# Performance work log

Measured on AMD Instinct MI355X. Metric: run time of the kernel, lower is better.

## Reference

```python
import jax, jax.numpy as jnp
import numpy as np

B, L, D, H = 2, 1000, 288, 8
DIM = D // H          # 36 per-head dim
DFF = 2 * D           # 576 conv-FFN hidden
KS = L // 4           # 250 sampled keys per query
NQ = L // 4           # 250 selected (active) queries
EPS = 1e-5


def _layernorm(x, g, b):
    mu = x.mean(-1, keepdims=True)
    var = ((x - mu) ** 2).mean(-1, keepdims=True)
    return (x - mu) * jax.lax.rsqrt(var + EPS) * g + b


def _prob_attention(q, k, v, index_key):
    # q,k,v: [b,h,L,dim]; index_key: [L, KS]
    b, h, l, dim = q.shape
    # sample KS keys per query row (gather): [b,h,L,KS,dim]
    k_samp = jnp.take(k, index_key, axis=2)
    # sampled scores: [b,h,L,KS]
    scores_samp = jnp.einsum('bhld,bhlkd->bhlk', q, k_samp)
    # sparsity measure M(q) = max - mean(over full l_key, as in source)
    measure = scores_samp.max(-1) - scores_samp.sum(-1) / l
    # top-NQ active queries per (b,h): [b,h,NQ]
    idx_q = jax.lax.top_k(measure, NQ)[1]
    q_sel = jnp.take_along_axis(q, idx_q[..., None], axis=2)  # [b,h,NQ,dim]
    sim = jnp.einsum('bhqd,bhkd->bhqk', q_sel, k) * (1.0 / np.sqrt(dim))
    attn = jax.nn.softmax(sim, axis=-1)
    out_sel = jnp.einsum('bhqk,bhkd->bhqd', attn, v)          # [b,h,NQ,dim]
    # lazy queries get mean(V); scatter active outputs in
    out = jnp.broadcast_to(v.mean(axis=2, keepdims=True), v.shape)
    bi = jnp.arange(b)[:, None, None]
    hi = jnp.arange(h)[None, :, None]
    out = out.at[bi, hi, idx_q].set(out_sel)
    return out  # [b,h,L,dim]


def reference(x, index_key, Wq, bq, Wk, bk, Wv, bv, W1, b1, W2, b2,
              ln1_g, ln1_b, ln2_g, ln2_b):
    b, l, d = x.shape
    # QKV projections -> [b,h,L,dim]
    q = (x @ Wq.T + bq).reshape(b, l, H, DIM).transpose(0, 2, 1, 3)
    k = (x @ Wk.T + bk).reshape(b, l, H, DIM).transpose(0, 2, 1, 3)
    v = (x @ Wv.T + bv).reshape(b, l, H, DIM).transpose(0, 2, 1, 3)
    attn = _prob_attention(q, k, v, index_key)
    attn = attn.transpose(0, 2, 1, 3).reshape(b, l, d)
    # residual + LN1 (dropout is identity in eval)
    h1 = _layernorm(x + attn, ln1_g, ln1_b)
    # conv FFN (kernel_size=1 conv == per-position linear), exact GELU
    f = jax.nn.gelu(h1 @ W1.T + b1, approximate=False)   # [b,l,DFF]
    f = jax.nn.gelu(f @ W2.T + b2, approximate=False)    # [b,l,d]
    return _layernorm(f + h1, ln2_g, ln2_b)


def setup_inputs() -> dict:
    key = jax.random.key(0)
    ks = jax.random.split(key, 10)
    s = 0.05
    return {
        'x': jax.random.normal(ks[0], (B, L, D), jnp.float32),
        'index_key': jax.random.randint(ks[1], (L, KS), 0, L),
        'Wq': jax.random.normal(ks[2], (D, D), jnp.float32) * s,
        'bq': jnp.zeros((D,), jnp.float32),
        'Wk': jax.random.normal(ks[3], (D, D), jnp.float32) * s,
        'bk': jnp.zeros((D,), jnp.float32),
        'Wv': jax.random.normal(ks[4], (D, D), jnp.float32) * s,
        'bv': jnp.zeros((D,), jnp.float32),
        'W1': jax.random.normal(ks[5], (DFF, D), jnp.float32) * s,
        'b1': jnp.zeros((DFF,), jnp.float32),
        'W2': jax.random.normal(ks[6], (D, DFF), jnp.float32) * s,
        'b2': jnp.zeros((D,), jnp.float32),
        'ln1_g': jnp.ones((D,), jnp.float32),
        'ln1_b': jnp.zeros((D,), jnp.float32),
        'ln2_g': jnp.ones((D,), jnp.float32),
        'ln2_b': jnp.zeros((D,), jnp.float32),
    }
```

## Files before the change

kernel.cpp:

```cpp
#include <hip/hip_runtime.h>
#include <hip/hip_bf16.h>
#include <math.h>

#define B_ 2
#define L_ 1000
#define D_ 288
#define H_ 8
#define DIM_ 36
#define DFF_ 576
#define KS_ 250
#define NQ_ 250
#define BH_ (B_ * H_)
#define EPS_ 1e-5f
#define PSTRIDE_ 40

__device__ __forceinline__ float gelu_exact(float x) {
    return 0.5f * x * (1.0f + erff(x * 0.70710678118654752f));
}

__device__ __forceinline__ float dot4(float4 a, float4 b) {
    return a.x * b.x + a.y * b.y + a.z * b.z + a.w * b.w;
}

__global__ __launch_bounds__(256) void qkv_transpose_kernel(
    const float* __restrict__ Wq, const float* __restrict__ Wk,
    const float* __restrict__ Wv,
    float* __restrict__ WqT, float* __restrict__ WkT, float* __restrict__ WvT)
{
    __shared__ float tile[32][33];
    const int m = blockIdx.x / 81;
    const int t = blockIdx.x % 81;
    const float* src = (m == 0) ? Wq : (m == 1) ? Wk : Wv;
    float* dst = (m == 0) ? WqT : (m == 1) ? WkT : WvT;
    const int ty0 = (t / 9) * 32, tx0 = (t % 9) * 32;
    const int tx = threadIdx.x & 31, ty = threadIdx.x >> 5;
#pragma unroll
    for (int i = 0; i < 4; i++)
        tile[ty + 8 * i][tx] = src[(size_t)(ty0 + ty + 8 * i) * D_ + tx0 + tx];
    __syncthreads();
#pragma unroll
    for (int i = 0; i < 4; i++)
        dst[(size_t)(tx0 + ty + 8 * i) * D_ + ty0 + tx] = tile[tx][ty + 8 * i];
}

__global__ __launch_bounds__(256) void ffn_transpose_kernel(
    const float* __restrict__ W1, const float* __restrict__ W2,
    float* __restrict__ W1T, float* __restrict__ W2T)
{
    __shared__ float tile[32][33];
    int t = blockIdx.x;
    const float* src; float* dst; int Rr, Cc, ntx;
    if (t < 162) { src = W1; dst = W1T; Rr = DFF_; Cc = D_; ntx = 9; }
    else { t -= 162; src = W2; dst = W2T; Rr = D_; Cc = DFF_; ntx = 18; }
    const int ty0 = (t / ntx) * 32, tx0 = (t % ntx) * 32;
    const int tx = threadIdx.x & 31, ty = threadIdx.x >> 5;
#pragma unroll
    for (int i = 0; i < 4; i++)
        tile[ty + 8 * i][tx] = src[(size_t)(ty0 + ty + 8 * i) * Cc + tx0 + tx];
    __syncthreads();
#pragma unroll
    for (int i = 0; i < 4; i++)
        dst[(size_t)(tx0 + ty + 8 * i) * Rr + ty0 + tx] = tile[tx][ty + 8 * i];
}

__global__ __launch_bounds__(256) void ktranspose_kernel(
    const float* __restrict__ K, float* __restrict__ KT)
{
    __shared__ float tile[32][33];
    const int t = blockIdx.x;
    const int bh = t >> 6;
    const int rem = t & 63;
    const int lt = rem >> 1, dt = rem & 1;
    const int l0 = lt * 32, d0 = dt * 32;
    const int tx = threadIdx.x & 31, ty = threadIdx.x >> 5;
    const float* Kb = K + (size_t)bh * L_ * DIM_;
    float* KTb = KT + (size_t)bh * DIM_ * L_;
#pragma unroll
    for (int i = 0; i < 4; i++) {
        int l = l0 + ty + 8 * i, d = d0 + tx;
        tile[ty + 8 * i][tx] = (l < L_ && d < DIM_) ? Kb[(size_t)l * DIM_ + d] : 0.f;
    }
    __syncthreads();
#pragma unroll
    for (int i = 0; i < 4; i++) {
        int d = d0 + ty + 8 * i, l = l0 + tx;
        if (d < DIM_ && l < L_) KTb[(size_t)d * L_ + l] = tile[tx][ty + 8 * i];
    }
}

__global__ __launch_bounds__(256) void qkvT2_kernel(
    const float* __restrict__ x,
    const float* __restrict__ WqT, const float* __restrict__ WkT,
    const float* __restrict__ WvT,
    const float* __restrict__ bq, const float* __restrict__ bk,
    const float* __restrict__ bv,
    float* __restrict__ Q, float* __restrict__ K, float* __restrict__ V)
{
    __shared__ float xsT[D_][4];
    const int base = blockIdx.x * 4;
    const int tid = threadIdx.x;

    for (int idx = tid; idx < 4 * D_; idx += 256) {
        int r = idx / D_, k = idx % D_;
        xsT[k][r] = x[(size_t)(base + r) * D_ + k];
    }
    __syncthreads();

    if (tid < 216) {
        const int gcol = 4 * tid;
        const int m = gcol / D_;
        const int c = gcol - m * D_;
        const float* WT = (m == 0) ? WqT : (m == 1) ? WkT : WvT;
        const float* bias = (m == 0) ? bq : (m == 1) ? bk : bv;
        float* outp = (m == 0) ? Q : (m == 1) ? K : V;

        float a[4][4];
#pragma unroll
        for (int j = 0; j < 4; j++) {
            float bv2 = bias[c + j];
#pragma unroll
            for (int r = 0; r < 4; r++) a[j][r] = bv2;
        }

        for (int k = 0; k < D_; k++) {
            float4 w = *(const float4*)(WT + (size_t)k * D_ + c);
            float4 xv = *(const float4*)&xsT[k][0];
            a[0][0] += w.x * xv.x; a[0][1] += w.x * xv.y; a[0][2] += w.x * xv.z; a[0][3] += w.x * xv.w;
            a[1][0] += w.y * xv.x; a[1][1] += w.y * xv.y; a[1][2] += w.y * xv.z; a[1][3] += w.y * xv.w;
            a[2][0] += w.z * xv.x; a[2][1] += w.z * xv.y; a[2][2] += w.z * xv.z; a[2][3] += w.z * xv.w;
            a[3][0] += w.w * xv.x; a[3][1] += w.w * xv.y; a[3][2] += w.w * xv.z; a[3][3] += w.w * xv.w;
        }

#pragma unroll
        for (int j = 0; j < 4; j++) {
            int col = c + j;
            int h = col / DIM_, dd = col % DIM_;
#pragma unroll
            for (int r = 0; r < 4; r++) {
                int row = base + r;
                int b = row / L_, l = row % L_;
                outp[((size_t)(b * H_ + h) * L_ + l) * DIM_ + dd] = a[j][r];
            }
        }
    }
}

__global__ __launch_bounds__(320) void qkv_kernel(
    const float* __restrict__ x,
    const float* __restrict__ Wq, const float* __restrict__ bq,
    const float* __restrict__ Wk, const float* __restrict__ bk,
    const float* __restrict__ Wv, const float* __restrict__ bv,
    float* __restrict__ Q, float* __restrict__ K, float* __restrict__ V)
{
    constexpr int R = 8;
    __shared__ float xs[R][D_];
    const int base = blockIdx.x * R;
    const int tid = threadIdx.x;

    const float4* xsrc = (const float4*)(x + (size_t)base * D_);
    float4* xdst = (float4*)&xs[0][0];
    for (int i = tid; i < R * D_ / 4; i += 320) xdst[i] = xsrc[i];
    __syncthreads();

    if (tid < D_) {
        const float4* wq4 = (const float4*)(Wq + (size_t)tid * D_);
        const float4* wk4 = (const float4*)(Wk + (size_t)tid * D_);
        const float4* wv4 = (const float4*)(Wv + (size_t)tid * D_);
        float aq[R], ak[R], av[R];
        float biasq = bq[tid], biask = bk[tid], biasv = bv[tid];
#pragma unroll
        for (int r = 0; r < R; r++) { aq[r] = biasq; ak[r] = biask; av[r] = biasv; }
        for (int d4 = 0; d4 < D_ / 4; d4++) {
            float4 wqv = wq4[d4], wkv = wk4[d4], wvv = wv4[d4];
#pragma unroll
            for (int r = 0; r < R; r++) {
                float4 hv = *(const float4*)&xs[r][d4 * 4];
                aq[r] += dot4(hv, wqv);
                ak[r] += dot4(hv, wkv);
                av[r] += dot4(hv, wvv);
            }
        }
        const int h = tid / DIM_, dd = tid % DIM_;
#pragma unroll
        for (int r = 0; r < R; r++) {
            int row = base + r;
            int b = row / L_, l = row % L_;
            size_t o = ((size_t)(b * H_ + h) * L_ + l) * DIM_ + dd;
            Q[o] = aq[r]; K[o] = ak[r]; V[o] = av[r];
        }
    }
}

__global__ __launch_bounds__(256) void vmean_kernel(
    const float* __restrict__ V, float* __restrict__ Vmean)
{
    const int bh = blockIdx.x;
    const int tid = threadIdx.x;
    __shared__ float red[7][DIM_];
    if (tid < 252) {
        int g = tid / DIM_, d = tid % DIM_;
        const float* base = V + (size_t)bh * L_ * DIM_;
        float s = 0.f;
        for (int l = g; l < L_; l += 7) s += base[l * DIM_ + d];
        red[g][d] = s;
    }
    __syncthreads();
    if (tid < DIM_) {
        float s = 0.f;
#pragma unroll
        for (int g = 0; g < 7; g++) s += red[g][tid];
        Vmean[bh * DIM_ + tid] = s * (1.0f / L_);
    }
}

__global__ __launch_bounds__(256) void score_measure3_kernel(
    const float* __restrict__ Q, const float* __restrict__ KT,
    const int* __restrict__ index_key, float* __restrict__ measure)
{
    constexpr int R = 8;
    __shared__ float qs[R][DIM_];
    __shared__ float st[R][1004];
    const int bh = blockIdx.x / 125;
    const int qt = blockIdx.x % 125;
    const int tid = threadIdx.x;

    if (tid < R * DIM_ / 4)
        ((float4*)&qs[0][0])[tid] =
            ((const float4*)(Q + ((size_t)bh * L_ + qt * R) * DIM_))[tid];
    __syncthreads();

    const float* KTb = KT + (size_t)bh * DIM_ * L_;
#pragma unroll
    for (int i = 0; i < 4; i++) {
        const int k = i * 256 + tid;
        if (k < L_) {
            float acc[R];
#pragma unroll
            for (int r = 0; r < R; r++) acc[r] = 0.f;
#pragma unroll
            for (int d4 = 0; d4 < DIM_ / 4; d4++) {
                float4 kv;
                kv.x = KTb[(size_t)(d4 * 4 + 0) * L_ + k];
                kv.y = KTb[(size_t)(d4 * 4 + 1) * L_ + k];
                kv.z = KTb[(size_t)(d4 * 4 + 2) * L_ + k];
                kv.w = KTb[(size_t)(d4 * 4 + 3) * L_ + k];
#pragma unroll
                for (int r = 0; r < R; r++)
                    acc[r] += dot4(*(const float4*)&qs[r][d4 * 4], kv);
            }
#pragma unroll
            for (int r = 0; r < R; r++) st[r][k] = acc[r];
        }
    }
    __syncthreads();

    const int r = tid >> 5;
    const int lane = tid & 31;
    const int l = qt * R + r;
    const int* ik = index_key + l * KS_;
    float mx = -1e30f, sm = 0.f;
    for (int s = lane; s < KS_; s += 32) {
        float v = st[r][ik[s]];
        mx = fmaxf(mx, v);
        sm += v;
    }
#pragma unroll
    for (int off = 16; off; off >>= 1) {
        mx = fmaxf(mx, __shfl_xor(mx, off));
        sm += __shfl_xor(sm, off);
    }
    if (lane == 0) measure[bh * L_ + l] = mx - sm * (1.0f / (float)L_);
}

__global__ __launch_bounds__(256) void measure_kernel(
    const float* __restrict__ Q, const float* __restrict__ K,
    const int* __restrict__ index_key, float* __restrict__ measure)
{
    const int w = threadIdx.x >> 6;
    const int lane = threadIdx.x & 63;
    const int wid = blockIdx.x * 4 + w;
    const int bh = wid / L_;
    const int l = wid % L_;

    const float4* qp = (const float4*)(Q + ((size_t)bh * L_ + l) * DIM_);
    float4 q[9];
#pragma unroll
    for (int i = 0; i < 9; i++) q[i] = qp[i];

    const int* ik = index_key + l * KS_;
    const float* Kb = K + (size_t)bh * L_ * DIM_;

    float mx = -1e30f, sm = 0.f;
#pragma unroll
    for (int s = lane; s < KS_; s += 64) {
        int kidx = ik[s];
        const float4* k4 = (const float4*)(Kb + (size_t)kidx * DIM_);
        float acc = 0.f;
#pragma unroll
        for (int i = 0; i < 9; i++) acc += dot4(q[i], k4[i]);
        mx = fmaxf(mx, acc);
        sm += acc;
    }
#pragma unroll
    for (int off = 32; off; off >>= 1) {
        mx = fmaxf(mx, __shfl_xor(mx, off));
        sm += __shfl_xor(sm, off);
    }
    if (lane == 0) measure[wid] = mx - sm * (1.0f / (float)L_);
}

__global__ __launch_bounds__(256) void topk_rank_kernel(
    const float* __restrict__ measure, int* __restrict__ qlist,
    int* __restrict__ slot_map)
{
    const int bh = blockIdx.x >> 2;
    const int quarter = blockIdx.x & 3;
    __shared__ float m[L_];
    for (int i = threadIdx.x; i < L_; i += 256) m[i] = measure[bh * L_ + i];
    __syncthreads();
    const int i = quarter * 250 + threadIdx.x;
    if (threadIdx.x < 250) {
        float mi = m[i];
        int rank = 0;
        for (int j = 0; j < L_; j++) {
            float mj = m[j];
            rank += (mj > mi) || (mj == mi && j < i);
        }
        if (rank < NQ_) qlist[bh * NQ_ + rank] = i;
        slot_map[bh * L_ + i] = (rank < NQ_) ? rank : -1;
    }
}

__global__ __launch_bounds__(256) void attn_part_kernel(
    const float* __restrict__ Q, const float* __restrict__ K,
    const float* __restrict__ V, const int* __restrict__ qlist,
    float* __restrict__ part, int nchunk, int chunk_len)
{
    const int bh = blockIdx.x / nchunk;
    const int chunk = blockIdx.x % nchunk;
    const int slot = threadIdx.x;
    if (slot >= NQ_) return;

    const int qidx = qlist[bh * NQ_ + slot];
    const float4* qp = (const float4*)(Q + ((size_t)bh * L_ + qidx) * DIM_);
    float4 q[9];
#pragma unroll
    for (int i = 0; i < 9; i++) q[i] = qp[i];

    const float* Kb = K + (size_t)bh * L_ * DIM_;
    const float* Vb = V + (size_t)bh * L_ * DIM_;
    const float scale = (float)(1.0 / 6.0);

    float4 acc[9];
#pragma unroll
    for (int i = 0; i < 9; i++) acc[i] = make_float4(0.f, 0.f, 0.f, 0.f);
    float sum = 0.f;

    const int k0 = chunk * chunk_len;
    for (int j = 0; j < chunk_len; j++) {
        const int key = k0 + j;
        const float4* kp = (const float4*)(Kb + (size_t)key * DIM_);
        float s = 0.f;
#pragma unroll
        for (int i = 0; i < 9; i++) s += dot4(q[i], kp[i]);
        float e = __expf(s * scale);
        sum += e;
        const float4* vp = (const float4*)(Vb + (size_t)key * DIM_);
#pragma unroll
        for (int i = 0; i < 9; i++) {
            float4 vv = vp[i];
            acc[i].x += e * vv.x;
            acc[i].y += e * vv.y;
            acc[i].z += e * vv.z;
            acc[i].w += e * vv.w;
        }
    }

    float* p = part + ((size_t)(bh * NQ_ + slot) * nchunk + chunk) * PSTRIDE_;
#pragma unroll
    for (int i = 0; i < 9; i++) ((float4*)p)[i] = acc[i];
    p[DIM_] = sum;
}

__global__ __launch_bounds__(256) void combine_all_kernel(
    const float* __restrict__ part, const int* __restrict__ slot_map,
    const float* __restrict__ Vmean, float* __restrict__ attn_out, int nchunk)
{
    int idx = blockIdx.x * blockDim.x + threadIdx.x;
    if (idx >= B_ * L_ * D_) return;
    int dfull = idx % D_;
    int bl = idx / D_;
    int b = bl / L_, l = bl % L_;
    int h = dfull / DIM_, d = dfull % DIM_;
    int bh = b * H_ + h;
    int slot = slot_map[bh * L_ + l];
    float v;
    if (slot < 0) {
        v = Vmean[bh * DIM_ + d];
    } else {
        const float* p = part + (size_t)(bh * NQ_ + slot) * nchunk * PSTRIDE_;
        float a = 0.f, s = 0.f;
        for (int c = 0; c < nchunk; c++) {
            a += p[c * PSTRIDE_ + d];
            s += p[c * PSTRIDE_ + DIM_];
        }
        v = a / s;
    }
    attn_out[idx] = v;
}

__global__ __launch_bounds__(64) void ln1_kernel(
    const float* __restrict__ x, const float* __restrict__ attn,
    const float* __restrict__ g, const float* __restrict__ bb,
    float* __restrict__ h1)
{
    const int row = blockIdx.x;
    const int lane = threadIdx.x;
    const float* xr = x + (size_t)row * D_;
    const float* ar = attn + (size_t)row * D_;

    float vals[5];
    float s = 0.f;
#pragma unroll
    for (int i = 0; i < 5; i++) {
        int j = lane + i * 64;
        float v = (j < D_) ? (xr[j] + ar[j]) : 0.f;
        vals[i] = v;
        s += v;
    }
#pragma unroll
    for (int off = 32; off; off >>= 1) s += __shfl_xor(s, off);
    float mu = s * (1.0f / D_);

    float vs = 0.f;
#pragma unroll
    for (int i = 0; i < 5; i++) {
        int j = lane + i * 64;
        if (j < D_) { float dd = vals[i] - mu; vs += dd * dd; }
    }
#pragma unroll
    for (int off = 32; off; off >>= 1) vs += __shfl_xor(vs, off);
    float rstd = rsqrtf(vs * (1.0f / D_) + EPS_);

#pragma unroll
    for (int i = 0; i < 5; i++) {
        int j = lane + i * 64;
        if (j < D_) h1[(size_t)row * D_ + j] = (vals[i] - mu) * rstd * g[j] + bb[j];
    }
}

__global__ __launch_bounds__(288) void ffn_fused2b_kernel(
    const float* __restrict__ h1,
    const float* __restrict__ W1T, const float* __restrict__ b1,
    const float* __restrict__ W2T, const float* __restrict__ b2,
    const float* __restrict__ g, const float* __restrict__ bb,
    float* __restrict__ out)
{
    __shared__ float hs[4][D_];
    __shared__ float fs[4][DFF_];
    __shared__ float red[3456];
    __shared__ float ys[4][D_];
    const int base = blockIdx.x * 4;
    const int tid = threadIdx.x;

    {
        const float4* src = (const float4*)(h1 + (size_t)base * D_);
        float4* dst = (float4*)&hs[0][0];
        for (int i = tid; i < 4 * D_ / 4; i += 288) dst[i] = src[i];
    }
    __syncthreads();

    {
        const int kg = tid / 144;
        const int ct = tid - kg * 144;
        const int c = 4 * ct;
        float a[4][4];
        if (kg == 0) {
#pragma unroll
            for (int j = 0; j < 4; j++) {
                float bv = b1[c + j];
#pragma unroll
                for (int r = 0; r < 4; r++) a[j][r] = bv;
            }
        } else {
#pragma unroll
            for (int j = 0; j < 4; j++)
#pragma unroll
                for (int r = 0; r < 4; r++) a[j][r] = 0.f;
        }
        const int kbeg = kg * 144;
        for (int k = kbeg; k < kbeg + 144; k++) {
            float4 w = *(const float4*)(W1T + (size_t)k * DFF_ + c);
            float x0 = hs[0][k], x1 = hs[1][k], x2 = hs[2][k], x3 = hs[3][k];
            a[0][0] += w.x * x0; a[0][1] += w.x * x1; a[0][2] += w.x * x2; a[0][3] += w.x * x3;
            a[1][0] += w.y * x0; a[1][1] += w.y * x1; a[1][2] += w.y * x2; a[1][3] += w.y * x3;
            a[2][0] += w.z * x0; a[2][1] += w.z * x1; a[2][2] += w.z * x2; a[2][3] += w.z * x3;
            a[3][0] += w.w * x0; a[3][1] += w.w * x1; a[3][2] += w.w * x2; a[3][3] += w.w * x3;
        }
        if (kg == 1) {
#pragma unroll
            for (int j = 0; j < 4; j++)
                *(float4*)&red[(j * 144 + ct) * 4] =
                    make_float4(a[j][0], a[j][1], a[j][2], a[j][3]);
        }
        __syncthreads();
        if (kg == 0) {
            float y[4][4];
#pragma unroll
            for (int j = 0; j < 4; j++) {
                float4 o = *(const float4*)&red[(j * 144 + ct) * 4];
                y[j][0] = gelu_exact(a[j][0] + o.x);
                y[j][1] = gelu_exact(a[j][1] + o.y);
                y[j][2] = gelu_exact(a[j][2] + o.z);
                y[j][3] = gelu_exact(a[j][3] + o.w);
            }
#pragma unroll
            for (int r = 0; r < 4; r++)
                *(float4*)&fs[r][c] = make_float4(y[0][r], y[1][r], y[2][r], y[3][r]);
        }
    }
    __syncthreads();

    {
        const int kg = tid / 72;
        const int ct = tid - kg * 72;
        const int c = 4 * ct;
        float a[4][4];
        if (kg == 0) {
#pragma unroll
            for (int j = 0; j < 4; j++) {
                float bv = b2[c + j];
#pragma unroll
                for (int r = 0; r < 4; r++) a[j][r] = bv;
            }
        } else {
#pragma unroll
            for (int j = 0; j < 4; j++)
#pragma unroll
                for (int r = 0; r < 4; r++) a[j][r] = 0.f;
        }
        const int kbeg = kg * 144;
        for (int k = kbeg; k < kbeg + 144; k++) {
            float4 w = *(const float4*)(W2T + (size_t)k * D_ + c);
            float f0 = fs[0][k], f1 = fs[1][k], f2 = fs[2][k], f3 = fs[3][k];
            a[0][0] += w.x * f0; a[0][1] += w.x * f1; a[0][2] += w.x * f2; a[0][3] += w.x * f3;
            a[1][0] += w.y * f0; a[1][1] += w.y * f1; a[1][2] += w.y * f2; a[1][3] += w.y * f3;
            a[2][0] += w.z * f0; a[2][1] += w.z * f1; a[2][2] += w.z * f2; a[2][3] += w.z * f3;
            a[3][0] += w.w * f0; a[3][1] += w.w * f1; a[3][2] += w.w * f2; a[3][3] += w.w * f3;
        }
        if (kg >= 1) {
#pragma unroll
            for (int j = 0; j < 4; j++)
                *(float4*)&red[(((kg - 1) * 4 + j) * 72 + ct) * 4] =
                    make_float4(a[j][0], a[j][1], a[j][2], a[j][3]);
        }
        __syncthreads();
        if (kg == 0) {
            float y[4][4];
#pragma unroll
            for (int j = 0; j < 4; j++) {
                float4 o0 = *(const float4*)&red[((0 * 4 + j) * 72 + ct) * 4];
                float4 o1 = *(const float4*)&red[((1 * 4 + j) * 72 + ct) * 4];
                float4 o2 = *(const float4*)&red[((2 * 4 + j) * 72 + ct) * 4];
                y[j][0] = gelu_exact(a[j][0] + o0.x + o1.x + o2.x) + hs[0][c + j];
                y[j][1] = gelu_exact(a[j][1] + o0.y + o1.y + o2.y) + hs[1][c + j];
                y[j][2] = gelu_exact(a[j][2] + o0.z + o1.z + o2.z) + hs[2][c + j];
                y[j][3] = gelu_exact(a[j][3] + o0.w + o1.w + o2.w) + hs[3][c + j];
            }
#pragma unroll
            for (int r = 0; r < 4; r++)
                *(float4*)&ys[r][c] = make_float4(y[0][r], y[1][r], y[2][r], y[3][r]);
        }
    }
    __syncthreads();

    const int w = tid >> 6;
    const int lane = tid & 63;
    if (w < 4) {
        const int r = w;
        float s = 0.f, ss = 0.f;
#pragma unroll
        for (int i = 0; i < 5; i++) {
            int j = lane + i * 64;
            if (j < D_) { float y = ys[r][j]; s += y; ss += y * y; }
        }
#pragma unroll
        for (int off = 32; off; off >>= 1) {
            s += __shfl_xor(s, off);
            ss += __shfl_xor(ss, off);
        }
        float mu = s * (1.0f / D_);
        float var = ss * (1.0f / D_) - mu * mu;
        float rstd = rsqrtf(var + EPS_);
        int row = base + r;
#pragma unroll
        for (int i = 0; i < 5; i++) {
            int j = lane + i * 64;
            if (j < D_) out[(size_t)row * D_ + j] = (ys[r][j] - mu) * rstd * g[j] + bb[j];
        }
    }
}

__global__ __launch_bounds__(192) void ffn1_kernel(
    const float* __restrict__ h1,
    const float* __restrict__ W1, const float* __restrict__ b1,
    float* __restrict__ f1)
{
    constexpr int R = 8;
    __shared__ float hs[R][D_];
    const int base = blockIdx.x * R;
    const int tid = threadIdx.x;

    const float4* hsrc = (const float4*)(h1 + (size_t)base * D_);
    float4* hdst = (float4*)&hs[0][0];
    for (int i = tid; i < R * D_ / 4; i += 192) hdst[i] = hsrc[i];
    __syncthreads();

    const int j0 = tid, j1 = tid + 192, j2 = tid + 384;
    const float4* w0 = (const float4*)(W1 + (size_t)j0 * D_);
    const float4* w1 = (const float4*)(W1 + (size_t)j1 * D_);
    const float4* w2 = (const float4*)(W1 + (size_t)j2 * D_);
    float a0[R], a1[R], a2[R];
    float bb0 = b1[j0], bb1 = b1[j1], bb2 = b1[j2];
#pragma unroll
    for (int r = 0; r < R; r++) { a0[r] = bb0; a1[r] = bb1; a2[r] = bb2; }

    for (int d4 = 0; d4 < D_ / 4; d4++) {
        float4 x0 = w0[d4], x1 = w1[d4], x2 = w2[d4];
#pragma unroll
        for (int r = 0; r < R; r++) {
            float4 hv = *(const float4*)&hs[r][d4 * 4];
            a0[r] += dot4(hv, x0);
            a1[r] += dot4(hv, x1);
            a2[r] += dot4(hv, x2);
        }
    }
#pragma unroll
    for (int r = 0; r < R; r++) {
        size_t rowo = (size_t)(base + r) * DFF_;
        f1[rowo + j0] = gelu_exact(a0[r]);
        f1[rowo + j1] = gelu_exact(a1[r]);
        f1[rowo + j2] = gelu_exact(a2[r]);
    }
}

__global__ __launch_bounds__(320) void ffn2_ln_kernel(
    const float* __restrict__ f1, const float* __restrict__ h1,
    const float* __restrict__ W2, const float* __restrict__ b2,
    const float* __restrict__ g, const float* __restrict__ bb,
    float* __restrict__ out)
{
    constexpr int R = 8;
    __shared__ float fs[R][DFF_];
    __shared__ float hs[R][D_];
    __shared__ float ys[R][D_];
    const int base = blockIdx.x * R;
    const int tid = threadIdx.x;

    const float4* fsrc = (const float4*)(f1 + (size_t)base * DFF_);
    float4* fdst = (float4*)&fs[0][0];
    for (int i = tid; i < R * DFF_ / 4; i += 320) fdst[i] = fsrc[i];
    const float4* hsrc = (const float4*)(h1 + (size_t)base * D_);
    float4* hdst = (float4*)&hs[0][0];
    for (int i = tid; i < R * D_ / 4; i += 320) hdst[i] = hsrc[i];
    __syncthreads();

    if (tid < D_) {
        const float4* w4 = (const float4*)(W2 + (size_t)tid * DFF_);
        float acc[R];
        float bias = b2[tid];
#pragma unroll
        for (int r = 0; r < R; r++) acc[r] = bias;
        for (int d4 = 0; d4 < DFF_ / 4; d4++) {
            float4 wv = w4[d4];
#pragma unroll
            for (int r = 0; r < R; r++) {
                float4 fv = *(const float4*)&fs[r][d4 * 4];
                acc[r] += dot4(fv, wv);
            }
        }
#pragma unroll
        for (int r = 0; r < R; r++) ys[r][tid] = gelu_exact(acc[r]) + hs[r][tid];
    }
    __syncthreads();

    const int w = tid >> 6;
    const int lane = tid & 63;
    for (int r = w; r < R; r += 5) {
        float s = 0.f, ss = 0.f;
#pragma unroll
        for (int i = 0; i < 5; i++) {
            int j = lane + i * 64;
            if (j < D_) { float y = ys[r][j]; s += y; ss += y * y; }
        }
#pragma unroll
        for (int off = 32; off; off >>= 1) {
            s += __shfl_xor(s, off);
            ss += __shfl_xor(ss, off);
        }
        float mu = s * (1.0f / D_);
        float var = ss * (1.0f / D_) - mu * mu;
        float rstd = rsqrtf(var + EPS_);
        int row = base + r;
#pragma unroll
        for (int i = 0; i < 5; i++) {
            int j = lane + i * 64;
            if (j < D_) out[(size_t)row * D_ + j] = (ys[r][j] - mu) * rstd * g[j] + bb[j];
        }
    }
}

extern "C" void kernel_launch(void* const* d_in, const int* in_sizes, int n_in,
                              void* d_out, int out_size, void* d_ws, size_t ws_size,
                              hipStream_t stream)
{
    const float* x         = (const float*)d_in[0];
    const int*   index_key = (const int*)  d_in[1];
    const float* Wq = (const float*)d_in[2];
    const float* bq = (const float*)d_in[3];
    const float* Wk = (const float*)d_in[4];
    const float* bk = (const float*)d_in[5];
    const float* Wv = (const float*)d_in[6];
    const float* bv = (const float*)d_in[7];
    const float* W1 = (const float*)d_in[8];
    const float* b1 = (const float*)d_in[9];
    const float* W2 = (const float*)d_in[10];
    const float* b2 = (const float*)d_in[11];
    const float* ln1_g = (const float*)d_in[12];
    const float* ln1_b = (const float*)d_in[13];
    const float* ln2_g = (const float*)d_in[14];
    const float* ln2_b = (const float*)d_in[15];
    float* out = (float*)d_out;

    float* Q        = (float*)d_ws;
    float* K        = Q + 576000;
    float* V        = K + 576000;
    float* Vmean    = V + 576000;
    float* measure  = Vmean + 576;
    float* attn_out = measure + 16000;
    float* h1       = attn_out + 576000;
    int*   qlist    = (int*)(h1 + 576000);
    int*   slot_map = qlist + 4000;
    float* part     = (float*)(slot_map + 16000);
    float* f1       = part;
    float* KT       = part + 4000000;

    float* WqT = part;
    float* WkT = WqT + 82944;
    float* WvT = WkT + 82944;
    float* W1T = part;
    float* W2T = part + 165888;

    const size_t kt_end = 2916576ull + 4000000ull + 576000ull;
    const bool   big    = ws_size >= kt_end * sizeof(float);
    const int    nchunk = big ? 25 : 8;
    const int    chunk_len = L_ / nchunk;

    if (big) {
        qkv_transpose_kernel<<<243, 256, 0, stream>>>(Wq, Wk, Wv, WqT, WkT, WvT);
        qkvT2_kernel<<<500, 256, 0, stream>>>(x, WqT, WkT, WvT, bq, bk, bv, Q, K, V);
    } else {
        qkv_kernel<<<250, 320, 0, stream>>>(x, Wq, bq, Wk, bk, Wv, bv, Q, K, V);
    }
    vmean_kernel<<<BH_, 256, 0, stream>>>(V, Vmean);
    if (big) {
        ktranspose_kernel<<<BH_ * 64, 256, 0, stream>>>(K, KT);
        score_measure3_kernel<<<BH_ * 125, 256, 0, stream>>>(Q, KT, index_key, measure);
    } else {
        measure_kernel<<<4000, 256, 0, stream>>>(Q, K, index_key, measure);
    }
    topk_rank_kernel<<<BH_ * 4, 256, 0, stream>>>(measure, qlist, slot_map);
    attn_part_kernel<<<BH_ * nchunk, 256, 0, stream>>>(Q, K, V, qlist, part, nchunk, chunk_len);
    combine_all_kernel<<<(B_ * L_ * D_ + 255) / 256, 256, 0, stream>>>(
        part, slot_map, Vmean, attn_out, nchunk);
    ln1_kernel<<<B_ * L_, 64, 0, stream>>>(x, attn_out, ln1_g, ln1_b, h1);
    if (big) {
        ffn_transpose_kernel<<<324, 256, 0, stream>>>(W1, W2, W1T, W2T);
        ffn_fused2b_kernel<<<500, 288, 0, stream>>>(h1, W1T, b1, W2T, b2, ln2_g, ln2_b, out);
    } else {
        ffn1_kernel<<<250, 192, 0, stream>>>(h1, W1, b1, f1);
        ffn2_ln_kernel<<<250, 320, 0, stream>>>(f1, h1, W2, b2, ln2_g, ln2_b, out);
    }
}
```

Measured before the change: 303.7 us.

## Fuse K transpose into QKV, merge topk with vmean and combine with LN1, stage attention K/V in LDS

The QKV projection now also writes the transposed K directly, which removes the separate K-transpose kernel. The V-mean reduction moves into the top-k ranking launch, and the partial-combine step is fused with LN1 into one per-row kernel. The attention-partial kernel stages each chunk's K and V in shared memory, and the fused FFN kernel processes 8 rows per block instead of 4. Together these cut kernel launches and global memory traffic, at the cost of more registers and shared memory per block and fewer FFN blocks.

```diff
diff --git a/kernel.cpp b/kernel.cpp
--- a/kernel.cpp
+++ b/kernel.cpp
@@ -1,5 +1,4 @@
 #include <hip/hip_runtime.h>
-#include <hip/hip_bf16.h>
 #include <math.h>
 
 #define B_ 2
@@ -13,6 +12,7 @@
 #define BH_ (B_ * H_)
 #define EPS_ 1e-5f
 #define PSTRIDE_ 40
+#define MAXCL_ 125
 
 __device__ __forceinline__ float gelu_exact(float x) {
     return 0.5f * x * (1.0f + erff(x * 0.70710678118654752f));
@@ -63,38 +63,14 @@
         dst[(size_t)(tx0 + ty + 8 * i) * Rr + ty0 + tx] = tile[tx][ty + 8 * i];
 }
 
-__global__ __launch_bounds__(256) void ktranspose_kernel(
-    const float* __restrict__ K, float* __restrict__ KT)
-{
-    __shared__ float tile[32][33];
-    const int t = blockIdx.x;
-    const int bh = t >> 6;
-    const int rem = t & 63;
-    const int lt = rem >> 1, dt = rem & 1;
-    const int l0 = lt * 32, d0 = dt * 32;
-    const int tx = threadIdx.x & 31, ty = threadIdx.x >> 5;
-    const float* Kb = K + (size_t)bh * L_ * DIM_;
-    float* KTb = KT + (size_t)bh * DIM_ * L_;
-#pragma unroll
-    for (int i = 0; i < 4; i++) {
-        int l = l0 + ty + 8 * i, d = d0 + tx;
-        tile[ty + 8 * i][tx] = (l < L_ && d < DIM_) ? Kb[(size_t)l * DIM_ + d] : 0.f;
-    }
-    __syncthreads();
-#pragma unroll
-    for (int i = 0; i < 4; i++) {
-        int d = d0 + ty + 8 * i, l = l0 + tx;
-        if (d < DIM_ && l < L_) KTb[(size_t)d * L_ + l] = tile[tx][ty + 8 * i];
-    }
-}
-
 __global__ __launch_bounds__(256) void qkvT2_kernel(
     const float* __restrict__ x,
     const float* __restrict__ WqT, const float* __restrict__ WkT,
     const float* __restrict__ WvT,
     const float* __restrict__ bq, const float* __restrict__ bk,
     const float* __restrict__ bv,
-    float* __restrict__ Q, float* __restrict__ K, float* __restrict__ V)
+    float* __restrict__ Q, float* __restrict__ K, float* __restrict__ V,
+    float* __restrict__ KT)
 {
     __shared__ float xsT[D_][4];
     const int base = blockIdx.x * 4;
@@ -131,6 +107,8 @@
             a[3][0] += w.w * xv.x; a[3][1] += w.w * xv.y; a[3][2] += w.w * xv.z; a[3][3] += w.w * xv.w;
         }
 
+        const int bb_ = base / L_;
+        const int l0 = base % L_;
 #pragma unroll
         for (int j = 0; j < 4; j++) {
             int col = c + j;
@@ -140,6 +118,10 @@
                 int row = base + r;
                 int b = row / L_, l = row % L_;
                 outp[((size_t)(b * H_ + h) * L_ + l) * DIM_ + dd] = a[j][r];
+            }
+            if (m == 1) {
+                *(float4*)(KT + ((size_t)(bb_ * H_ + h) * DIM_ + dd) * L_ + l0) =
+                    make_float4(a[j][0], a[j][1], a[j][2], a[j][3]);
             }
         }
     }
@@ -188,28 +170,6 @@
             size_t o = ((size_t)(b * H_ + h) * L_ + l) * DIM_ + dd;
             Q[o] = aq[r]; K[o] = ak[r]; V[o] = av[r];
         }
-    }
-}
-
-__global__ __launch_bounds__(256) void vmean_kernel(
-    const float* __restrict__ V, float* __restrict__ Vmean)
-{
-    const int bh = blockIdx.x;
-    const int tid = threadIdx.x;
-    __shared__ float red[7][DIM_];
-    if (tid < 252) {
-        int g = tid / DIM_, d = tid % DIM_;
-        const float* base = V + (size_t)bh * L_ * DIM_;
-        float s = 0.f;
-        for (int l = g; l < L_; l += 7) s += base[l * DIM_ + d];
-        red[g][d] = s;
-    }
-    __syncthreads();
-    if (tid < DIM_) {
-        float s = 0.f;
-#pragma unroll
-        for (int g = 0; g < 7; g++) s += red[g][tid];
-        Vmean[bh * DIM_ + tid] = s * (1.0f / L_);
     }
 }
 
@@ -309,36 +269,73 @@
     if (lane == 0) measure[wid] = mx - sm * (1.0f / (float)L_);
 }
 
-__global__ __launch_bounds__(256) void topk_rank_kernel(
+__global__ __launch_bounds__(256) void topk_vmean_kernel(
     const float* __restrict__ measure, int* __restrict__ qlist,
-    int* __restrict__ slot_map)
-{
-    const int bh = blockIdx.x >> 2;
-    const int quarter = blockIdx.x & 3;
-    __shared__ float m[L_];
-    for (int i = threadIdx.x; i < L_; i += 256) m[i] = measure[bh * L_ + i];
-    __syncthreads();
-    const int i = quarter * 250 + threadIdx.x;
-    if (threadIdx.x < 250) {
-        float mi = m[i];
-        int rank = 0;
-        for (int j = 0; j < L_; j++) {
-            float mj = m[j];
-            rank += (mj > mi) || (mj == mi && j < i);
-        }
-        if (rank < NQ_) qlist[bh * NQ_ + rank] = i;
-        slot_map[bh * L_ + i] = (rank < NQ_) ? rank : -1;
-    }
-}
-
-__global__ __launch_bounds__(256) void attn_part_kernel(
+    int* __restrict__ slot_map, const float* __restrict__ V,
+    float* __restrict__ Vmean)
+{
+    if (blockIdx.x < BH_ * 4) {
+        const int bh = blockIdx.x >> 2;
+        const int quarter = blockIdx.x & 3;
+        __shared__ float m[L_];
+        for (int i = threadIdx.x; i < L_; i += 256) m[i] = measure[bh * L_ + i];
+        __syncthreads();
+        const int i = quarter * 250 + threadIdx.x;
+        if (threadIdx.x < 250) {
+            float mi = m[i];
+            int rank = 0;
+            for (int j = 0; j < L_; j++) {
+                float mj = m[j];
+                rank += (mj > mi) || (mj == mi && j < i);
+            }
+            if (rank < NQ_) qlist[bh * NQ_ + rank] = i;
+            slot_map[bh * L_ + i] = (rank < NQ_) ? rank : -1;
+        }
+    } else {
+        const int bh = blockIdx.x - BH_ * 4;
+        const int tid = threadIdx.x;
+        __shared__ float red2[7][DIM_];
+        if (tid < 252) {
+            int gq = tid / DIM_, d = tid % DIM_;
+            const float* basep = V + (size_t)bh * L_ * DIM_;
+            float s = 0.f;
+            for (int l = gq; l < L_; l += 7) s += basep[l * DIM_ + d];
+            red2[gq][d] = s;
+        }
+        __syncthreads();
+        if (tid < DIM_) {
+            float s = 0.f;
+#pragma unroll
+            for (int gq = 0; gq < 7; gq++) s += red2[gq][tid];
+            Vmean[bh * DIM_ + tid] = s * (1.0f / L_);
+        }
+    }
+}
+
+__global__ __launch_bounds__(256) void attn_part2_kernel(
     const float* __restrict__ Q, const float* __restrict__ K,
     const float* __restrict__ V, const int* __restrict__ qlist,
     float* __restrict__ part, int nchunk, int chunk_len)
 {
+    __shared__ float Ks[MAXCL_ * DIM_];
+    __shared__ float Vs[MAXCL_ * DIM_];
     const int bh = blockIdx.x / nchunk;
     const int chunk = blockIdx.x % nchunk;
-    const int slot = threadIdx.x;
+    const int tid = threadIdx.x;
+    const int k0 = chunk * chunk_len;
+
+    {
+        const float4* Ksrc = (const float4*)(K + ((size_t)bh * L_ + k0) * DIM_);
+        const float4* Vsrc = (const float4*)(V + ((size_t)bh * L_ + k0) * DIM_);
+        const int nf4 = chunk_len * (DIM_ / 4);
+        for (int i = tid; i < nf4; i += 256) {
+            ((float4*)Ks)[i] = Ksrc[i];
+            ((float4*)Vs)[i] = Vsrc[i];
+        }
+    }
+    __syncthreads();
+
+    const int slot = tid;
     if (slot >= NQ_) return;
 
     const int qidx = qlist[bh * NQ_ + slot];
@@ -347,25 +344,20 @@
 #pragma unroll
     for (int i = 0; i < 9; i++) q[i] = qp[i];
 
-    const float* Kb = K + (size_t)bh * L_ * DIM_;
-    const float* Vb = V + (size_t)bh * L_ * DIM_;
     const float scale = (float)(1.0 / 6.0);
-
     float4 acc[9];
 #pragma unroll
     for (int i = 0; i < 9; i++) acc[i] = make_float4(0.f, 0.f, 0.f, 0.f);
     float sum = 0.f;
 
-    const int k0 = chunk * chunk_len;
     for (int j = 0; j < chunk_len; j++) {
-        const int key = k0 + j;
-        const float4* kp = (const float4*)(Kb + (size_t)key * DIM_);
+        const float4* kp = (const float4*)(Ks + j * DIM_);
         float s = 0.f;
 #pragma unroll
         for (int i = 0; i < 9; i++) s += dot4(q[i], kp[i]);
         float e = __expf(s * scale);
         sum += e;
-        const float4* vp = (const float4*)(Vb + (size_t)key * DIM_);
+        const float4* vp = (const float4*)(Vs + j * DIM_);
 #pragma unroll
         for (int i = 0; i < 9; i++) {
             float4 vv = vp[i];
@@ -382,91 +374,75 @@
     p[DIM_] = sum;
 }
 
-__global__ __launch_bounds__(256) void combine_all_kernel(
-    const float* __restrict__ part, const int* __restrict__ slot_map,
-    const float* __restrict__ Vmean, float* __restrict__ attn_out, int nchunk)
-{
-    int idx = blockIdx.x * blockDim.x + threadIdx.x;
-    if (idx >= B_ * L_ * D_) return;
-    int dfull = idx % D_;
-    int bl = idx / D_;
-    int b = bl / L_, l = bl % L_;
-    int h = dfull / DIM_, d = dfull % DIM_;
-    int bh = b * H_ + h;
-    int slot = slot_map[bh * L_ + l];
-    float v;
-    if (slot < 0) {
-        v = Vmean[bh * DIM_ + d];
-    } else {
-        const float* p = part + (size_t)(bh * NQ_ + slot) * nchunk * PSTRIDE_;
-        float a = 0.f, s = 0.f;
-        for (int c = 0; c < nchunk; c++) {
-            a += p[c * PSTRIDE_ + d];
-            s += p[c * PSTRIDE_ + DIM_];
-        }
-        v = a / s;
-    }
-    attn_out[idx] = v;
-}
-
-__global__ __launch_bounds__(64) void ln1_kernel(
-    const float* __restrict__ x, const float* __restrict__ attn,
+__global__ __launch_bounds__(320) void combine_ln1_kernel(
+    const float* __restrict__ x, const float* __restrict__ part,
+    const int* __restrict__ slot_map, const float* __restrict__ Vmean,
     const float* __restrict__ g, const float* __restrict__ bb,
-    float* __restrict__ h1)
+    float* __restrict__ h1, int nchunk)
 {
     const int row = blockIdx.x;
-    const int lane = threadIdx.x;
-    const float* xr = x + (size_t)row * D_;
-    const float* ar = attn + (size_t)row * D_;
-
-    float vals[5];
-    float s = 0.f;
-#pragma unroll
-    for (int i = 0; i < 5; i++) {
-        int j = lane + i * 64;
-        float v = (j < D_) ? (xr[j] + ar[j]) : 0.f;
-        vals[i] = v;
-        s += v;
-    }
-#pragma unroll
-    for (int off = 32; off; off >>= 1) s += __shfl_xor(s, off);
-    float mu = s * (1.0f / D_);
-
-    float vs = 0.f;
-#pragma unroll
-    for (int i = 0; i < 5; i++) {
-        int j = lane + i * 64;
-        if (j < D_) { float dd = vals[i] - mu; vs += dd * dd; }
-    }
-#pragma unroll
-    for (int off = 32; off; off >>= 1) vs += __shfl_xor(vs, off);
-    float rstd = rsqrtf(vs * (1.0f / D_) + EPS_);
-
-#pragma unroll
-    for (int i = 0; i < 5; i++) {
-        int j = lane + i * 64;
-        if (j < D_) h1[(size_t)row * D_ + j] = (vals[i] - mu) * rstd * g[j] + bb[j];
-    }
-}
-
-__global__ __launch_bounds__(288) void ffn_fused2b_kernel(
+    const int b = row / L_, l = row % L_;
+    const int tid = threadIdx.x;
+    __shared__ float psum[5], pssq[5];
+
+    float y = 0.f;
+    if (tid < D_) {
+        const int h = tid / DIM_, d = tid % DIM_;
+        const int bh = b * H_ + h;
+        const int slot = slot_map[bh * L_ + l];
+        float v;
+        if (slot < 0) {
+            v = Vmean[bh * DIM_ + d];
+        } else {
+            const float* p = part + (size_t)(bh * NQ_ + slot) * nchunk * PSTRIDE_;
+            float a = 0.f, s = 0.f;
+            for (int c = 0; c < nchunk; c++) {
+                a += p[c * PSTRIDE_ + d];
+                s += p[c * PSTRIDE_ + DIM_];
+            }
+            v = a / s;
+        }
+        y = x[(size_t)row * D_ + tid] + v;
+    }
+
+    float s1 = y, s2 = y * y;
+#pragma unroll
+    for (int off = 32; off; off >>= 1) {
+        s1 += __shfl_xor(s1, off);
+        s2 += __shfl_xor(s2, off);
+    }
+    const int w = tid >> 6, lane = tid & 63;
+    if (lane == 0) { psum[w] = s1; pssq[w] = s2; }
+    __syncthreads();
+    float ts = 0.f, tq = 0.f;
+#pragma unroll
+    for (int i = 0; i < 5; i++) { ts += psum[i]; tq += pssq[i]; }
+    float mu = ts * (1.0f / D_);
+    float var = tq * (1.0f / D_) - mu * mu;
+    float rstd = rsqrtf(var + EPS_);
+    if (tid < D_)
+        h1[(size_t)row * D_ + tid] = (y - mu) * rstd * g[tid] + bb[tid];
+}
+
+__global__ __launch_bounds__(288) void ffn_fused3_kernel(
     const float* __restrict__ h1,
     const float* __restrict__ W1T, const float* __restrict__ b1,
     const float* __restrict__ W2T, const float* __restrict__ b2,
     const float* __restrict__ g, const float* __restrict__ bb,
     float* __restrict__ out)
 {
-    __shared__ float hs[4][D_];
-    __shared__ float fs[4][DFF_];
-    __shared__ float red[3456];
-    __shared__ float ys[4][D_];
-    const int base = blockIdx.x * 4;
+    constexpr int R = 8;
+    __shared__ float hs[R][D_];
+    __shared__ float fs[R][DFF_];
+    __shared__ float red[6912];
+    __shared__ float ys[R][D_];
+    const int base = blockIdx.x * R;
     const int tid = threadIdx.x;
 
     {
         const float4* src = (const float4*)(h1 + (size_t)base * D_);
         float4* dst = (float4*)&hs[0][0];
-        for (int i = tid; i < 4 * D_ / 4; i += 288) dst[i] = src[i];
+        for (int i = tid; i < R * D_ / 4; i += 288) dst[i] = src[i];
     }
     __syncthreads();
 
@@ -474,48 +450,52 @@
         const int kg = tid / 144;
         const int ct = tid - kg * 144;
         const int c = 4 * ct;
-        float a[4][4];
-        if (kg == 0) {
-#pragma unroll
-            for (int j = 0; j < 4; j++) {
-                float bv = b1[c + j];
-#pragma unroll
-                for (int r = 0; r < 4; r++) a[j][r] = bv;
-            }
-        } else {
-#pragma unroll
-            for (int j = 0; j < 4; j++)
-#pragma unroll
-                for (int r = 0; r < 4; r++) a[j][r] = 0.f;
+        float a[4][R];
+#pragma unroll
+        for (int j = 0; j < 4; j++) {
+            float bv = (kg == 0) ? b1[c + j] : 0.f;
+#pragma unroll
+            for (int r = 0; r < R; r++) a[j][r] = bv;
         }
         const int kbeg = kg * 144;
         for (int k = kbeg; k < kbeg + 144; k++) {
             float4 w = *(const float4*)(W1T + (size_t)k * DFF_ + c);
-            float x0 = hs[0][k], x1 = hs[1][k], x2 = hs[2][k], x3 = hs[3][k];
-            a[0][0] += w.x * x0; a[0][1] += w.x * x1; a[0][2] += w.x * x2; a[0][3] += w.x * x3;
-            a[1][0] += w.y * x0; a[1][1] += w.y * x1; a[1][2] += w.y * x2; a[1][3] += w.y * x3;
-            a[2][0] += w.z * x0; a[2][1] += w.z * x1; a[2][2] += w.z * x2; a[2][3] += w.z * x3;
-            a[3][0] += w.w * x0; a[3][1] += w.w * x1; a[3][2] += w.w * x2; a[3][3] += w.w * x3;
+#pragma unroll
+            for (int r = 0; r < R; r++) {
+                float xv = hs[r][k];
+                a[0][r] += w.x * xv;
+                a[1][r] += w.y * xv;
+                a[2][r] += w.z * xv;
+                a[3][r] += w.w * xv;
+            }
         }
         if (kg == 1) {
 #pragma unroll
-            for (int j = 0; j < 4; j++)
-                *(float4*)&red[(j * 144 + ct) * 4] =
+            for (int j = 0; j < 4; j++) {
+                *(float4*)&red[(j * 144 + ct) * 8 + 0] =
                     make_float4(a[j][0], a[j][1], a[j][2], a[j][3]);
+                *(float4*)&red[(j * 144 + ct) * 8 + 4] =
+                    make_float4(a[j][4], a[j][5], a[j][6], a[j][7]);
+            }
         }
         __syncthreads();
         if (kg == 0) {
-            float y[4][4];
+            float y[4][R];
 #pragma unroll
             for (int j = 0; j < 4; j++) {
-                float4 o = *(const float4*)&red[(j * 144 + ct) * 4];
-                y[j][0] = gelu_exact(a[j][0] + o.x);
-                y[j][1] = gelu_exact(a[j][1] + o.y);
-                y[j][2] = gelu_exact(a[j][2] + o.z);
-                y[j][3] = gelu_exact(a[j][3] + o.w);
-            }
-#pragma unroll
-            for (int r = 0; r < 4; r++)
+                float4 o0 = *(const float4*)&red[(j * 144 + ct) * 8 + 0];
+                float4 o1 = *(const float4*)&red[(j * 144 + ct) * 8 + 4];
+                y[j][0] = gelu_exact(a[j][0] + o0.x);
+                y[j][1] = gelu_exact(a[j][1] + o0.y);
+                y[j][2] = gelu_exact(a[j][2] + o0.z);
+                y[j][3] = gelu_exact(a[j][3] + o0.w);
+                y[j][4] = gelu_exact(a[j][4] + o1.x);
+                y[j][5] = gelu_exact(a[j][5] + o1.y);
+                y[j][6] = gelu_exact(a[j][6] + o1.z);
+                y[j][7] = gelu_exact(a[j][7] + o1.w);
+            }
+#pragma unroll
+            for (int r = 0; r < R; r++)
                 *(float4*)&fs[r][c] = make_float4(y[0][r], y[1][r], y[2][r], y[3][r]);
         }
     }
@@ -525,50 +505,52 @@
         const int kg = tid / 72;
         const int ct = tid - kg * 72;
         const int c = 4 * ct;
-        float a[4][4];
-        if (kg == 0) {
-#pragma unroll
-            for (int j = 0; j < 4; j++) {
-                float bv = b2[c + j];
-#pragma unroll
-                for (int r = 0; r < 4; r++) a[j][r] = bv;
-            }
-        } else {
-#pragma unroll
-            for (int j = 0; j < 4; j++)
-#pragma unroll
-                for (int r = 0; r < 4; r++) a[j][r] = 0.f;
+        float a[4][R];
+#pragma unroll
+        for (int j = 0; j < 4; j++) {
+            float bv = (kg == 0) ? b2[c + j] : 0.f;
+#pragma unroll
+            for (int r = 0; r < R; r++) a[j][r] = bv;
         }
         const int kbeg = kg * 144;
         for (int k = kbeg; k < kbeg + 144; k++) {
             float4 w = *(const float4*)(W2T + (size_t)k * D_ + c);
-            float f0 = fs[0][k], f1 = fs[1][k], f2 = fs[2][k], f3 = fs[3][k];
-            a[0][0] += w.x * f0; a[0][1] += w.x * f1; a[0][2] += w.x * f2; a[0][3] += w.x * f3;
-            a[1][0] += w.y * f0; a[1][1] += w.y * f1; a[1][2] += w.y * f2; a[1][3] += w.y * f3;
-            a[2][0] += w.z * f0; a[2][1] += w.z * f1; a[2][2] += w.z * f2; a[2][3] += w.z * f3;
-            a[3][0] += w.w * f0; a[3][1] += w.w * f1; a[3][2] += w.w * f2; a[3][3] += w.w * f3;
+#pragma unroll
+            for (int r = 0; r < R; r++) {
+                float fv = fs[r][k];
+                a[0][r] += w.x * fv;
+                a[1][r] += w.y * fv;
+                a[2][r] += w.z * fv;
+                a[3][r] += w.w * fv;
+            }
         }
         if (kg >= 1) {
 #pragma unroll
-            for (int j = 0; j < 4; j++)
-                *(float4*)&red[(((kg - 1) * 4 + j) * 72 + ct) * 4] =
+            for (int j = 0; j < 4; j++) {
+                *(float4*)&red[(((kg - 1) * 4 + j) * 72 + ct) * 8 + 0] =
                     make_float4(a[j][0], a[j][1], a[j][2], a[j][3]);
+                *(float4*)&red[(((kg - 1) * 4 + j) * 72 + ct) * 8 + 4] =
+                    make_float4(a[j][4], a[j][5], a[j][6], a[j][7]);
+            }
         }
         __syncthreads();
         if (kg == 0) {
-            float y[4][4];
+            float y[4][R];
 #pragma unroll
             for (int j = 0; j < 4; j++) {
-                float4 o0 = *(const float4*)&red[((0 * 4 + j) * 72 + ct) * 4];
-                float4 o1 = *(const float4*)&red[((1 * 4 + j) * 72 + ct) * 4];
-                float4 o2 = *(const float4*)&red[((2 * 4 + j) * 72 + ct) * 4];
-                y[j][0] = gelu_exact(a[j][0] + o0.x + o1.x + o2.x) + hs[0][c + j];
-                y[j][1] = gelu_exact(a[j][1] + o0.y + o1.y + o2.y) + hs[1][c + j];
-                y[j][2] = gelu_exact(a[j][2] + o0.z + o1.z + o2.z) + hs[2][c + j];
-                y[j][3] = gelu_exact(a[j][3] + o0.w + o1.w + o2.w) + hs[3][c + j];
-            }
-#pragma unroll
-            for (int r = 0; r < 4; r++)
+#pragma unroll
+                for (int rq = 0; rq < 2; rq++) {
+                    float4 o0 = *(const float4*)&red[((0 * 4 + j) * 72 + ct) * 8 + rq * 4];
+                    float4 o1 = *(const float4*)&red[((1 * 4 + j) * 72 + ct) * 8 + rq * 4];
+                    float4 o2 = *(const float4*)&red[((2 * 4 + j) * 72 + ct) * 8 + rq * 4];
+                    y[j][rq * 4 + 0] = gelu_exact(a[j][rq * 4 + 0] + o0.x + o1.x + o2.x) + hs[rq * 4 + 0][c + j];
+                    y[j][rq * 4 + 1] = gelu_exact(a[j][rq * 4 + 1] + o0.y + o1.y + o2.y) + hs[rq * 4 + 1][c + j];
+                    y[j][rq * 4 + 2] = gelu_exact(a[j][rq * 4 + 2] + o0.z + o1.z + o2.z) + hs[rq * 4 + 2][c + j];
+                    y[j][rq * 4 + 3] = gelu_exact(a[j][rq * 4 + 3] + o0.w + o1.w + o2.w) + hs[rq * 4 + 3][c + j];
+                }
+            }
+#pragma unroll
+            for (int r = 0; r < R; r++)
                 *(float4*)&ys[r][c] = make_float4(y[0][r], y[1][r], y[2][r], y[3][r]);
         }
     }
@@ -577,26 +559,30 @@
     const int w = tid >> 6;
     const int lane = tid & 63;
     if (w < 4) {
-        const int r = w;
-        float s = 0.f, ss = 0.f;
-#pragma unroll
-        for (int i = 0; i < 5; i++) {
-            int j = lane + i * 64;
-            if (j < D_) { float y = ys[r][j]; s += y; ss += y * y; }
-        }
-#pragma unroll
-        for (int off = 32; off; off >>= 1) {
-            s += __shfl_xor(s, off);
-            ss += __shfl_xor(ss, off);
-        }
-        float mu = s * (1.0f / D_);
-        float var = ss * (1.0f / D_) - mu * mu;
-        float rstd = rsqrtf(var + EPS_);
-        int row = base + r;
-#pragma unroll
-        for (int i = 0; i < 5; i++) {
-            int j = lane + i * 64;
-            if (j < D_) out[(size_t)row * D_ + j] = (ys[r][j] - mu) * rstd * g[j] + bb[j];
+#pragma unroll
+        for (int rr = 0; rr < 2; rr++) {
+            const int r = w * 2 + rr;
+            float s = 0.f, ss = 0.f;
+#pragma unroll
+            for (int i = 0; i < 5; i++) {
+                int j = lane + i * 64;
+                if (j < D_) { float yv = ys[r][j]; s += yv; ss += yv * yv; }
+            }
+#pragma unroll
+            for (int off = 32; off; off >>= 1) {
+                s += __shfl_xor(s, off);
+                ss += __shfl_xor(ss, off);
+            }
+            float mu = s * (1.0f / D_);
+            float var = ss * (1.0f / D_) - mu * mu;
+            float rstd = rsqrtf(var + EPS_);
+            int row = base + r;
+#pragma unroll
+            for (int i = 0; i < 5; i++) {
+                int j = lane + i * 64;
+                if (j < D_)
+                    out[(size_t)row * D_ + j] = (ys[r][j] - mu) * rstd * g[j] + bb[j];
+            }
         }
     }
 }
@@ -758,25 +744,19 @@
 
     if (big) {
         qkv_transpose_kernel<<<243, 256, 0, stream>>>(Wq, Wk, Wv, WqT, WkT, WvT);
-        qkvT2_kernel<<<500, 256, 0, stream>>>(x, WqT, WkT, WvT, bq, bk, bv, Q, K, V);
+        qkvT2_kernel<<<500, 256, 0, stream>>>(x, WqT, WkT, WvT, bq, bk, bv, Q, K, V, KT);
+        score_measure3_kernel<<<BH_ * 125, 256, 0, stream>>>(Q, KT, index_key, measure);
     } else {
         qkv_kernel<<<250, 320, 0, stream>>>(x, Wq, bq, Wk, bk, Wv, bv, Q, K, V);
-    }
-    vmean_kernel<<<BH_, 256, 0, stream>>>(V, Vmean);
-    if (big) {
-        ktranspose_kernel<<<BH_ * 64, 256, 0, stream>>>(K, KT);
-        score_measure3_kernel<<<BH_ * 125, 256, 0, stream>>>(Q, KT, index_key, measure);
-    } else {
         measure_kernel<<<4000, 256, 0, stream>>>(Q, K, index_key, measure);
     }
-    topk_rank_kernel<<<BH_ * 4, 256, 0, stream>>>(measure, qlist, slot_map);
-    attn_part_kernel<<<BH_ * nchunk, 256, 0, stream>>>(Q, K, V, qlist, part, nchunk, chunk_len);
-    combine_all_kernel<<<(B_ * L_ * D_ + 255) / 256, 256, 0, stream>>>(
-        part, slot_map, Vmean, attn_out, nchunk);
-    ln1_kernel<<<B_ * L_, 64, 0, stream>>>(x, attn_out, ln1_g, ln1_b, h1);
+    topk_vmean_kernel<<<BH_ * 4 + BH_, 256, 0, stream>>>(measure, qlist, slot_map, V, Vmean);
+    attn_part2_kernel<<<BH_ * nchunk, 256, 0, stream>>>(Q, K, V, qlist, part, nchunk, chunk_len);
+    combine_ln1_kernel<<<B_ * L_, 320, 0, stream>>>(x, part, slot_map, Vmean,
+                                                    ln1_g, ln1_b, h1, nchunk);
     if (big) {
         ffn_transpose_kernel<<<324, 256, 0, stream>>>(W1, W2, W1T, W2T);
-        ffn_fused2b_kernel<<<500, 288, 0, stream>>>(h1, W1T, b1, W2T, b2, ln2_g, ln2_b, out);
+        ffn_fused3_kernel<<<250, 288, 0, stream>>>(h1, W1T, b1, W2T, b2, ln2_g, ln2_b, out);
     } else {
         ffn1_kernel<<<250, 192, 0, stream>>>(h1, W1, b1, f1);
         ffn2_ln_kernel<<<250, 320, 0, stream>>>(f1, h1, W2, b2, ln2_g, ln2_b, out);
```

After: 273.2 us. 10.0% less time.
